# Performance work log

Hardware: AMD Instinct MI355X
Metric: run time of the kernel (lower is better)

The kernel has to match this reference:

```python
import jax, jax.numpy as jnp
import numpy as np

B, N, DIM, HID = 128, 4096, 16, 128

def _linear_init(key, fan_in, fan_out):
    # torch nn.Linear default: U(-1/sqrt(fan_in), 1/sqrt(fan_in))
    kw, kb = jax.random.split(key)
    bound = 1.0 / np.sqrt(fan_in)
    W = jax.random.uniform(kw, (fan_in, fan_out), minval=-bound, maxval=bound, dtype=jnp.float32)
    b = jax.random.uniform(kb, (fan_out,), minval=-bound, maxval=bound, dtype=jnp.float32)
    return W, b

def setup_inputs() -> dict:
    key = jax.random.key(0)
    ks = jax.random.split(key, 8)
    x = jax.random.normal(ks[0], (B, N, DIM), dtype=jnp.float32)
    adj_col = (jax.random.uniform(ks[1], (N,), dtype=jnp.float32) > 0.5).astype(jnp.float32)
    W_n2e, b_n2e = _linear_init(ks[2], 2 * DIM, HID)
    W_e2e, b_e2e = _linear_init(ks[3], HID, HID)
    W_e2n, b_e2n = _linear_init(ks[4], HID, HID)
    W_n2n, b_n2n = _linear_init(ks[5], HID, HID)
    W_out, b_out = _linear_init(ks[6], DIM + HID, DIM)
    return {"x": x, "adj_col": adj_col,
            "W_n2e": W_n2e, "b_n2e": b_n2e,
            "W_e2e": W_e2e, "b_e2e": b_e2e,
            "W_e2n": W_e2n, "b_e2n": b_e2n,
            "W_n2n": W_n2n, "b_n2n": b_n2n,
            "W_out": W_out, "b_out": b_out,
            "i": 0}

def reference(x, adj_col, W_n2e, b_n2e, W_e2e, b_e2e, W_e2n, b_e2n, W_n2n, b_n2n, W_out, b_out, i):
    starter = x                                        # [B, N, dim]
    ender = x[:, i, :][:, None, :]                     # [B, 1, dim]
    ender = jnp.broadcast_to(ender, starter.shape)     # [B, N, dim]
    h = jnp.concatenate([starter, ender], axis=2)      # [B, N, 2*dim]
    h = jax.nn.relu(h @ W_n2e + b_n2e)                 # [B, N, hid]
    h = jax.nn.relu(h @ W_e2e + b_e2e)                 # [B, N, hid]
    h = h * adj_col[None, :, None]                     # adjacency mask
    h = jnp.sum(h, axis=1)                             # [B, hid]
    h = jax.nn.relu(h @ W_e2n + b_e2n)
    h = jax.nn.relu(h @ W_n2n + b_n2n)
    h = jnp.concatenate([starter[:, i, :], h], axis=-1)  # [B, dim+hid]
    return h @ W_out + b_out                           # [B, dim]
```

## Files before the change

### kernel.cpp

```cpp
#include <hip/hip_runtime.h>
#include <hip/hip_bf16.h>

#define B_    128
#define N_    4096
#define DIM_  16
#define HID_  128
#define ROWS_ 512
#define CHUNK_ 128
#define NCH_  (ROWS_ / CHUNK_)

typedef __bf16 bf16x8 __attribute__((ext_vector_type(8)));
typedef float floatx16 __attribute__((ext_vector_type(16)));

__device__ inline bf16x8 load_cvt8(const float* __restrict__ p) {
  const float4 u = *(const float4*)p;
  const float4 v = *(const float4*)(p + 4);
  bf16x8 r;
  r[0] = (__bf16)u.x; r[1] = (__bf16)u.y; r[2] = (__bf16)u.z; r[3] = (__bf16)u.w;
  r[4] = (__bf16)v.x; r[5] = (__bf16)v.y; r[6] = (__bf16)v.z; r[7] = (__bf16)v.w;
  return r;
}

__global__ __launch_bounds__(256, 2) void edge_kernel(
    const float* __restrict__ x, const float* __restrict__ adj,
    const float* __restrict__ W1, const float* __restrict__ b1,
    const float* __restrict__ W2, const float* __restrict__ b2,
    const int* __restrict__ ip, float* __restrict__ accg)
{
  __shared__ __align__(16) __bf16 sW1T[HID_][24];
  __shared__ __align__(16) __bf16 sW2T[HID_][136];
  __shared__ __align__(16) __bf16 sH1[CHUNK_][136];
  __shared__ float sB1[HID_], sB2[HID_], sAcc[HID_], sEnder[DIM_];

  const int t  = threadIdx.x;
  const int b  = blockIdx.y;
  const int n0 = blockIdx.x * ROWS_;
  const int ii = __ldg(ip);

  if (t < DIM_) sEnder[t] = x[((size_t)b * N_ + ii) * DIM_ + t];
  for (int e = t; e < DIM_ * HID_; e += 256) {
    int k = e >> 7, n = e & 127;
    sW1T[n][k] = (__bf16)W1[k * HID_ + n];
  }
  for (int e = t; e < HID_ * HID_; e += 256) {
    int k = e >> 7, n = e & 127;
    sW2T[n][k] = (__bf16)W2[k * HID_ + n];
  }
  __syncthreads();
  if (t < HID_) {
    float s = b1[t];
    #pragma unroll
    for (int k = 0; k < DIM_; ++k) s += sEnder[k] * W1[(DIM_ + k) * HID_ + t];
    sB1[t] = s;
    sB2[t] = b2[t];
    sAcc[t] = 0.f;
  }

  const int wave = t >> 6, lane = t & 63;
  const int half = lane >> 5, l31 = lane & 31;
  const int rt0 = (wave >> 1) << 1;
  const int ct0 = (wave & 1) << 1;
  const int col0 = ct0 * 32 + l31, col1 = col0 + 32;

  for (int c = 0; c < NCH_; ++c) {
    const int nb = n0 + c * CHUNK_;
    __syncthreads();

    {
      bf16x8 bf0 = *(const bf16x8*)&sW1T[col0][half * 8];
      bf16x8 bf1 = *(const bf16x8*)&sW1T[col1][half * 8];
      const float bv0 = sB1[col0], bv1 = sB1[col1];
      #pragma unroll
      for (int dr = 0; dr < 2; ++dr) {
        const int rt = rt0 + dr;
        bf16x8 af = load_cvt8(&x[((size_t)b * N_ + nb + rt * 32 + l31) * DIM_ + half * 8]);
        floatx16 a0, a1;
        #pragma unroll
        for (int r = 0; r < 16; ++r) { a0[r] = bv0; a1[r] = bv1; }
        a0 = __builtin_amdgcn_mfma_f32_32x32x16_bf16(af, bf0, a0, 0, 0, 0);
        a1 = __builtin_amdgcn_mfma_f32_32x32x16_bf16(af, bf1, a1, 0, 0, 0);
        #pragma unroll
        for (int r = 0; r < 16; ++r) {
          const int row = rt * 32 + (r & 3) + ((r >> 2) << 3) + (half << 2);
          sH1[row][col0] = (__bf16)fmaxf(a0[r], 0.f);
          sH1[row][col1] = (__bf16)fmaxf(a1[r], 0.f);
        }
      }
    }
    __syncthreads();

    {
      floatx16 c00, c01, c10, c11;
      const float bv0 = sB2[col0], bv1 = sB2[col1];
      #pragma unroll
      for (int r = 0; r < 16; ++r) { c00[r] = bv0; c01[r] = bv1; c10[r] = bv0; c11[r] = bv1; }
      #pragma unroll
      for (int ks = 0; ks < 8; ++ks) {
        const int ko = ks * 16 + half * 8;
        bf16x8 A0 = *(const bf16x8*)&sH1[rt0 * 32      + l31][ko];
        bf16x8 A1 = *(const bf16x8*)&sH1[rt0 * 32 + 32 + l31][ko];
        bf16x8 B0 = *(const bf16x8*)&sW2T[col0][ko];
        bf16x8 B1 = *(const bf16x8*)&sW2T[col1][ko];
        c00 = __builtin_amdgcn_mfma_f32_32x32x16_bf16(A0, B0, c00, 0, 0, 0);
        c01 = __builtin_amdgcn_mfma_f32_32x32x16_bf16(A0, B1, c01, 0, 0, 0);
        c10 = __builtin_amdgcn_mfma_f32_32x32x16_bf16(A1, B0, c10, 0, 0, 0);
        c11 = __builtin_amdgcn_mfma_f32_32x32x16_bf16(A1, B1, c11, 0, 0, 0);
      }
      float p0 = 0.f, p1 = 0.f;
      #pragma unroll
      for (int g = 0; g < 4; ++g) {
        const float4 m0 = *(const float4*)&adj[nb + rt0 * 32      + (half << 2) + (g << 3)];
        const float4 m1 = *(const float4*)&adj[nb + rt0 * 32 + 32 + (half << 2) + (g << 3)];
        p0 += fmaxf(c00[4*g+0], 0.f) * m0.x + fmaxf(c00[4*g+1], 0.f) * m0.y
            + fmaxf(c00[4*g+2], 0.f) * m0.z + fmaxf(c00[4*g+3], 0.f) * m0.w;
        p0 += fmaxf(c10[4*g+0], 0.f) * m1.x + fmaxf(c10[4*g+1], 0.f) * m1.y
            + fmaxf(c10[4*g+2], 0.f) * m1.z + fmaxf(c10[4*g+3], 0.f) * m1.w;
        p1 += fmaxf(c01[4*g+0], 0.f) * m0.x + fmaxf(c01[4*g+1], 0.f) * m0.y
            + fmaxf(c01[4*g+2], 0.f) * m0.z + fmaxf(c01[4*g+3], 0.f) * m0.w;
        p1 += fmaxf(c11[4*g+0], 0.f) * m1.x + fmaxf(c11[4*g+1], 0.f) * m1.y
            + fmaxf(c11[4*g+2], 0.f) * m1.z + fmaxf(c11[4*g+3], 0.f) * m1.w;
      }
      atomicAdd(&sAcc[col0], p0);
      atomicAdd(&sAcc[col1], p1);
    }
  }
  __syncthreads();
  if (t < HID_) atomicAdd(&accg[b * HID_ + t], sAcc[t]);
}

__global__ void tail_kernel(
    const float* __restrict__ x, const float* __restrict__ acc,
    const float* __restrict__ W3, const float* __restrict__ b3,
    const float* __restrict__ W4, const float* __restrict__ b4,
    const float* __restrict__ W5, const float* __restrict__ b5,
    const int* __restrict__ ip, float* __restrict__ out)
{
  const int b = blockIdx.x, t = threadIdx.x;
  __shared__ float s0[HID_], s1[HID_], s2[HID_], se[DIM_];
  const int ii = __ldg(ip);
  if (t < DIM_) se[t] = x[((size_t)b * N_ + ii) * DIM_ + t];
  s0[t] = acc[b * HID_ + t];
  __syncthreads();
  float v = b3[t];
  for (int k = 0; k < HID_; ++k) v += s0[k] * W3[k * HID_ + t];
  s1[t] = fmaxf(v, 0.f);
  __syncthreads();
  float w = b4[t];
  for (int k = 0; k < HID_; ++k) w += s1[k] * W4[k * HID_ + t];
  s2[t] = fmaxf(w, 0.f);
  __syncthreads();
  if (t < DIM_) {
    float o = b5[t];
    #pragma unroll
    for (int k = 0; k < DIM_; ++k) o += se[k] * W5[k * DIM_ + t];
    for (int k = 0; k < HID_; ++k) o += s2[k] * W5[(DIM_ + k) * DIM_ + t];
    out[b * DIM_ + t] = o;
  }
}

extern "C" void kernel_launch(void* const* d_in, const int* in_sizes, int n_in,
                              void* d_out, int out_size, void* d_ws, size_t ws_size,
                              hipStream_t stream) {
  const float* x   = (const float*)d_in[0];
  const float* adj = (const float*)d_in[1];
  const float* W1  = (const float*)d_in[2];
  const float* b1  = (const float*)d_in[3];
  const float* W2  = (const float*)d_in[4];
  const float* b2  = (const float*)d_in[5];
  const float* W3  = (const float*)d_in[6];
  const float* b3  = (const float*)d_in[7];
  const float* W4  = (const float*)d_in[8];
  const float* b4  = (const float*)d_in[9];
  const float* W5  = (const float*)d_in[10];
  const float* b5  = (const float*)d_in[11];
  const int*   ip  = (const int*)d_in[12];
  float* out  = (float*)d_out;
  float* accg = (float*)d_ws;

  hipMemsetAsync(accg, 0, B_ * HID_ * sizeof(float), stream);
  edge_kernel<<<dim3(N_ / ROWS_, B_), 256, 0, stream>>>(x, adj, W1, b1, W2, b2, ip, accg);
  tail_kernel<<<B_, HID_, 0, stream>>>(x, accg, W3, b3, W4, b4, W5, b5, ip, out);
}
```

Measured before the change: 146.1 us.

## Compact masked rows, keep W2 in registers, and replace global atomics with partials

Each block compacts the indices of rows whose adjacency is nonzero and runs both MLP layers only on those rows, padding the last chunk and masking its tail in the reduction. This skips the work for rows the mask would zero out. The W2 fragments move from shared memory into registers, sH1 writes are packed as bf16 pairs through a permuted W1 column order, and occupancy is raised to three blocks per CU. The global atomicAdd plus memset is replaced by per-tile partial sums that the tail kernel adds up. The cost is higher register pressure, atomics used to build the shared index list, and a gather on x.

```diff
diff --git a/kernel.cpp b/kernel.cpp
--- a/kernel.cpp
+++ b/kernel.cpp
@@ -7,8 +7,9 @@
 #define HID_  128
 #define ROWS_ 512
 #define CHUNK_ 128
-#define NCH_  (ROWS_ / CHUNK_)
-
+#define NTILE_ (N_ / ROWS_)
+
+typedef __bf16 bf16x2 __attribute__((ext_vector_type(2)));
 typedef __bf16 bf16x8 __attribute__((ext_vector_type(8)));
 typedef float floatx16 __attribute__((ext_vector_type(16)));
 
@@ -21,115 +22,144 @@
   return r;
 }
 
-__global__ __launch_bounds__(256, 2) void edge_kernel(
+__global__ __launch_bounds__(256, 3) void edge_kernel(
     const float* __restrict__ x, const float* __restrict__ adj,
     const float* __restrict__ W1, const float* __restrict__ b1,
     const float* __restrict__ W2, const float* __restrict__ b2,
-    const int* __restrict__ ip, float* __restrict__ accg)
+    const int* __restrict__ ip, float* __restrict__ part)
 {
   __shared__ __align__(16) __bf16 sW1T[HID_][24];
-  __shared__ __align__(16) __bf16 sW2T[HID_][136];
   __shared__ __align__(16) __bf16 sH1[CHUNK_][136];
-  __shared__ float sB1[HID_], sB2[HID_], sAcc[HID_], sEnder[DIM_];
+  __shared__ float sB1[HID_];
+  __shared__ float sAcc[HID_];
+  __shared__ float sEnder[DIM_];
+  __shared__ int   sIdx[ROWS_];
+  __shared__ int   sCnt;
 
   const int t  = threadIdx.x;
   const int b  = blockIdx.y;
   const int n0 = blockIdx.x * ROWS_;
   const int ii = __ldg(ip);
 
+  if (t == 0) sCnt = 0;
   if (t < DIM_) sEnder[t] = x[((size_t)b * N_ + ii) * DIM_ + t];
+  __syncthreads();
+
+  #pragma unroll
+  for (int r = t; r < ROWS_; r += 256)
+    if (adj[n0 + r] != 0.f) sIdx[atomicAdd(&sCnt, 1)] = n0 + r;
+
   for (int e = t; e < DIM_ * HID_; e += 256) {
-    int k = e >> 7, n = e & 127;
-    sW1T[n][k] = (__bf16)W1[k * HID_ + n];
-  }
-  for (int e = t; e < HID_ * HID_; e += 256) {
-    int k = e >> 7, n = e & 127;
-    sW2T[n][k] = (__bf16)W2[k * HID_ + n];
-  }
-  __syncthreads();
+    int s = e & 127, k = e >> 7;
+    int c = s >> 5, n = s & 31;
+    int f = ((c >> 1) << 6) + 2 * n + (c & 1);
+    sW1T[s][k] = (__bf16)W1[k * HID_ + f];
+  }
+  __syncthreads();
+  const int cnt = sCnt;
+  const int nch = (cnt + CHUNK_ - 1) / CHUNK_;
+  for (int p = cnt + t; p < nch * CHUNK_; p += 256) sIdx[p] = n0;
   if (t < HID_) {
-    float s = b1[t];
-    #pragma unroll
-    for (int k = 0; k < DIM_; ++k) s += sEnder[k] * W1[(DIM_ + k) * HID_ + t];
+    int c = t >> 5, n = t & 31;
+    int f = ((c >> 1) << 6) + 2 * n + (c & 1);
+    float s = b1[f];
+    #pragma unroll
+    for (int k = 0; k < DIM_; ++k) s += sEnder[k] * W1[(DIM_ + k) * HID_ + f];
     sB1[t] = s;
-    sB2[t] = b2[t];
     sAcc[t] = 0.f;
   }
 
   const int wave = t >> 6, lane = t & 63;
   const int half = lane >> 5, l31 = lane & 31;
   const int rt0 = (wave >> 1) << 1;
-  const int ct0 = (wave & 1) << 1;
-  const int col0 = ct0 * 32 + l31, col1 = col0 + 32;
-
-  for (int c = 0; c < NCH_; ++c) {
-    const int nb = n0 + c * CHUNK_;
+  const int p4  = wave & 1;
+  const int col0 = p4 * 64 + l31, col1 = col0 + 32;
+  const int sc0  = p4 * 64 + 2 * l31;
+
+  bf16x8 w2a[8], w2b[8];
+  #pragma unroll
+  for (int s = 0; s < 8; ++s) {
+    const int kb = s * 16 + half * 8;
+    bf16x8 fa, fb;
+    #pragma unroll
+    for (int j = 0; j < 8; ++j) {
+      fa[j] = (__bf16)W2[(kb + j) * HID_ + col0];
+      fb[j] = (__bf16)W2[(kb + j) * HID_ + col1];
+    }
+    w2a[s] = fa; w2b[s] = fb;
+  }
+  const float bv0 = b2[col0], bv1 = b2[col1];
+  __syncthreads();
+
+  const bf16x8 bf0 = *(const bf16x8*)&sW1T[p4 * 64      + l31][half * 8];
+  const bf16x8 bf1 = *(const bf16x8*)&sW1T[p4 * 64 + 32 + l31][half * 8];
+  const float bva0 = sB1[p4 * 64 + l31], bva1 = sB1[p4 * 64 + 32 + l31];
+
+  float p0 = 0.f, p1 = 0.f;
+
+  for (int c = 0; c < nch; ++c) {
+    const int cb = c * CHUNK_;
     __syncthreads();
 
-    {
-      bf16x8 bf0 = *(const bf16x8*)&sW1T[col0][half * 8];
-      bf16x8 bf1 = *(const bf16x8*)&sW1T[col1][half * 8];
-      const float bv0 = sB1[col0], bv1 = sB1[col1];
-      #pragma unroll
-      for (int dr = 0; dr < 2; ++dr) {
-        const int rt = rt0 + dr;
-        bf16x8 af = load_cvt8(&x[((size_t)b * N_ + nb + rt * 32 + l31) * DIM_ + half * 8]);
-        floatx16 a0, a1;
-        #pragma unroll
-        for (int r = 0; r < 16; ++r) { a0[r] = bv0; a1[r] = bv1; }
-        a0 = __builtin_amdgcn_mfma_f32_32x32x16_bf16(af, bf0, a0, 0, 0, 0);
-        a1 = __builtin_amdgcn_mfma_f32_32x32x16_bf16(af, bf1, a1, 0, 0, 0);
-        #pragma unroll
-        for (int r = 0; r < 16; ++r) {
-          const int row = rt * 32 + (r & 3) + ((r >> 2) << 3) + (half << 2);
-          sH1[row][col0] = (__bf16)fmaxf(a0[r], 0.f);
-          sH1[row][col1] = (__bf16)fmaxf(a1[r], 0.f);
-        }
+    #pragma unroll
+    for (int dr = 0; dr < 2; ++dr) {
+      const int rt = rt0 + dr;
+      const int idx = sIdx[cb + rt * 32 + l31];
+      const bf16x8 af = load_cvt8(&x[((size_t)b * N_ + idx) * DIM_ + half * 8]);
+      floatx16 a0, a1;
+      #pragma unroll
+      for (int r = 0; r < 16; ++r) { a0[r] = bva0; a1[r] = bva1; }
+      a0 = __builtin_amdgcn_mfma_f32_32x32x16_bf16(af, bf0, a0, 0, 0, 0);
+      a1 = __builtin_amdgcn_mfma_f32_32x32x16_bf16(af, bf1, a1, 0, 0, 0);
+      #pragma unroll
+      for (int r = 0; r < 16; ++r) {
+        const int row = rt * 32 + (r & 3) + ((r >> 2) << 3) + (half << 2);
+        bf16x2 pv;
+        pv[0] = (__bf16)fmaxf(a0[r], 0.f);
+        pv[1] = (__bf16)fmaxf(a1[r], 0.f);
+        *(bf16x2*)&sH1[row][sc0] = pv;
       }
     }
     __syncthreads();
 
-    {
-      floatx16 c00, c01, c10, c11;
-      const float bv0 = sB2[col0], bv1 = sB2[col1];
-      #pragma unroll
-      for (int r = 0; r < 16; ++r) { c00[r] = bv0; c01[r] = bv1; c10[r] = bv0; c11[r] = bv1; }
-      #pragma unroll
-      for (int ks = 0; ks < 8; ++ks) {
-        const int ko = ks * 16 + half * 8;
-        bf16x8 A0 = *(const bf16x8*)&sH1[rt0 * 32      + l31][ko];
-        bf16x8 A1 = *(const bf16x8*)&sH1[rt0 * 32 + 32 + l31][ko];
-        bf16x8 B0 = *(const bf16x8*)&sW2T[col0][ko];
-        bf16x8 B1 = *(const bf16x8*)&sW2T[col1][ko];
-        c00 = __builtin_amdgcn_mfma_f32_32x32x16_bf16(A0, B0, c00, 0, 0, 0);
-        c01 = __builtin_amdgcn_mfma_f32_32x32x16_bf16(A0, B1, c01, 0, 0, 0);
-        c10 = __builtin_amdgcn_mfma_f32_32x32x16_bf16(A1, B0, c10, 0, 0, 0);
-        c11 = __builtin_amdgcn_mfma_f32_32x32x16_bf16(A1, B1, c11, 0, 0, 0);
+    floatx16 c00, c01, c10, c11;
+    #pragma unroll
+    for (int r = 0; r < 16; ++r) { c00[r] = bv0; c01[r] = bv1; c10[r] = bv0; c11[r] = bv1; }
+    #pragma unroll
+    for (int s = 0; s < 8; ++s) {
+      const int ko = s * 16 + half * 8;
+      const bf16x8 A0 = *(const bf16x8*)&sH1[rt0 * 32      + l31][ko];
+      const bf16x8 A1 = *(const bf16x8*)&sH1[rt0 * 32 + 32 + l31][ko];
+      c00 = __builtin_amdgcn_mfma_f32_32x32x16_bf16(A0, w2a[s], c00, 0, 0, 0);
+      c01 = __builtin_amdgcn_mfma_f32_32x32x16_bf16(A0, w2b[s], c01, 0, 0, 0);
+      c10 = __builtin_amdgcn_mfma_f32_32x32x16_bf16(A1, w2a[s], c10, 0, 0, 0);
+      c11 = __builtin_amdgcn_mfma_f32_32x32x16_bf16(A1, w2b[s], c11, 0, 0, 0);
+    }
+    if (cb + CHUNK_ <= cnt) {
+      #pragma unroll
+      for (int r = 0; r < 16; ++r) {
+        p0 += fmaxf(c00[r], 0.f) + fmaxf(c10[r], 0.f);
+        p1 += fmaxf(c01[r], 0.f) + fmaxf(c11[r], 0.f);
       }
-      float p0 = 0.f, p1 = 0.f;
-      #pragma unroll
-      for (int g = 0; g < 4; ++g) {
-        const float4 m0 = *(const float4*)&adj[nb + rt0 * 32      + (half << 2) + (g << 3)];
-        const float4 m1 = *(const float4*)&adj[nb + rt0 * 32 + 32 + (half << 2) + (g << 3)];
-        p0 += fmaxf(c00[4*g+0], 0.f) * m0.x + fmaxf(c00[4*g+1], 0.f) * m0.y
-            + fmaxf(c00[4*g+2], 0.f) * m0.z + fmaxf(c00[4*g+3], 0.f) * m0.w;
-        p0 += fmaxf(c10[4*g+0], 0.f) * m1.x + fmaxf(c10[4*g+1], 0.f) * m1.y
-            + fmaxf(c10[4*g+2], 0.f) * m1.z + fmaxf(c10[4*g+3], 0.f) * m1.w;
-        p1 += fmaxf(c01[4*g+0], 0.f) * m0.x + fmaxf(c01[4*g+1], 0.f) * m0.y
-            + fmaxf(c01[4*g+2], 0.f) * m0.z + fmaxf(c01[4*g+3], 0.f) * m0.w;
-        p1 += fmaxf(c11[4*g+0], 0.f) * m1.x + fmaxf(c11[4*g+1], 0.f) * m1.y
-            + fmaxf(c11[4*g+2], 0.f) * m1.z + fmaxf(c11[4*g+3], 0.f) * m1.w;
+    } else {
+      #pragma unroll
+      for (int r = 0; r < 16; ++r) {
+        const int q0 = cb + rt0 * 32 + (r & 3) + ((r >> 2) << 3) + (half << 2);
+        const int q1 = q0 + 32;
+        if (q0 < cnt) { p0 += fmaxf(c00[r], 0.f); p1 += fmaxf(c01[r], 0.f); }
+        if (q1 < cnt) { p0 += fmaxf(c10[r], 0.f); p1 += fmaxf(c11[r], 0.f); }
       }
-      atomicAdd(&sAcc[col0], p0);
-      atomicAdd(&sAcc[col1], p1);
-    }
-  }
-  __syncthreads();
-  if (t < HID_) atomicAdd(&accg[b * HID_ + t], sAcc[t]);
+    }
+  }
+
+  atomicAdd(&sAcc[col0], p0);
+  atomicAdd(&sAcc[col1], p1);
+  __syncthreads();
+  if (t < HID_) part[((size_t)b * NTILE_ + blockIdx.x) * HID_ + t] = sAcc[t];
 }
 
 __global__ void tail_kernel(
-    const float* __restrict__ x, const float* __restrict__ acc,
+    const float* __restrict__ x, const float* __restrict__ part,
     const float* __restrict__ W3, const float* __restrict__ b3,
     const float* __restrict__ W4, const float* __restrict__ b4,
     const float* __restrict__ W5, const float* __restrict__ b5,
@@ -139,13 +169,18 @@
   __shared__ float s0[HID_], s1[HID_], s2[HID_], se[DIM_];
   const int ii = __ldg(ip);
   if (t < DIM_) se[t] = x[((size_t)b * N_ + ii) * DIM_ + t];
-  s0[t] = acc[b * HID_ + t];
+  float a = 0.f;
+  #pragma unroll
+  for (int p = 0; p < NTILE_; ++p) a += part[((size_t)b * NTILE_ + p) * HID_ + t];
+  s0[t] = a;
   __syncthreads();
   float v = b3[t];
+  #pragma unroll 16
   for (int k = 0; k < HID_; ++k) v += s0[k] * W3[k * HID_ + t];
   s1[t] = fmaxf(v, 0.f);
   __syncthreads();
   float w = b4[t];
+  #pragma unroll 16
   for (int k = 0; k < HID_; ++k) w += s1[k] * W4[k * HID_ + t];
   s2[t] = fmaxf(w, 0.f);
   __syncthreads();
@@ -153,6 +188,7 @@
     float o = b5[t];
     #pragma unroll
     for (int k = 0; k < DIM_; ++k) o += se[k] * W5[k * DIM_ + t];
+    #pragma unroll 16
     for (int k = 0; k < HID_; ++k) o += s2[k] * W5[(DIM_ + k) * DIM_ + t];
     out[b * DIM_ + t] = o;
   }
@@ -175,9 +211,8 @@
   const float* b5  = (const float*)d_in[11];
   const int*   ip  = (const int*)d_in[12];
   float* out  = (float*)d_out;
-  float* accg = (float*)d_ws;
-
-  hipMemsetAsync(accg, 0, B_ * HID_ * sizeof(float), stream);
-  edge_kernel<<<dim3(N_ / ROWS_, B_), 256, 0, stream>>>(x, adj, W1, b1, W2, b2, ip, accg);
-  tail_kernel<<<B_, HID_, 0, stream>>>(x, accg, W3, b3, W4, b4, W5, b5, ip, out);
-}
+  float* part = (float*)d_ws;
+
+  edge_kernel<<<dim3(NTILE_, B_), 256, 0, stream>>>(x, adj, W1, b1, W2, b2, ip, part);
+  tail_kernel<<<B_, HID_, 0, stream>>>(x, part, W3, b3, W4, b4, W5, b5, ip, out);
+}
```

After: 199.3 us. 1.36x slower.
